# Kernel tuning notes

Hardware: AMD Instinct MI355X
Metric: run time of the kernel (lower is better)

Reference implementation:

```python
import jax, jax.numpy as jnp
import numpy as np

EPS = 1e-5
HEADS = 8
DIM_HEAD = 64
SCALE = DIM_HEAD ** -0.5
DEPTH = 4


def _layernorm(x, g, b):
    mu = jnp.mean(x, axis=-1, keepdims=True)
    var = jnp.var(x, axis=-1, keepdims=True)
    return (x - mu) * jax.lax.rsqrt(var + EPS) * g + b


def setup_inputs() -> dict:
    key = jax.random.key(0)
    ks = jax.random.split(key, 8)
    b, n, dim, mlp = 4, 1024, 512, 2048
    inner = HEADS * DIM_HEAD
    D = DEPTH
    s = 0.02  # realistic init scale
    return {
        "x": jax.random.normal(ks[0], (b, n, dim), jnp.float32),
        "ln1_g": jnp.ones((D, dim), jnp.float32),
        "ln1_b": jnp.zeros((D, dim), jnp.float32),
        "w_qkv": jax.random.normal(ks[1], (D, dim, 3 * inner), jnp.float32) * s,
        "reattn_w": jax.random.normal(ks[2], (D, HEADS, HEADS), jnp.float32),
        "rln_g": jnp.ones((D, HEADS), jnp.float32),
        "rln_b": jnp.zeros((D, HEADS), jnp.float32),
        "w_out": jax.random.normal(ks[3], (D, inner, dim), jnp.float32) * s,
        "b_out": jnp.zeros((D, dim), jnp.float32),
        "ln2_g": jnp.ones((D, dim), jnp.float32),
        "ln2_b": jnp.zeros((D, dim), jnp.float32),
        "w1": jax.random.normal(ks[4], (D, dim, mlp), jnp.float32) * s,
        "b1": jnp.zeros((D, mlp), jnp.float32),
        "w2": jax.random.normal(ks[5], (D, mlp, dim), jnp.float32) * s,
        "b2": jnp.zeros((D, dim), jnp.float32),
    }


def _attention(x, ln_g, ln_b, w_qkv, rw, rg, rb, w_out, b_out):
    b, n, dim = x.shape
    h, d = HEADS, DIM_HEAD
    hn = _layernorm(x, ln_g, ln_b)
    qkv = hn @ w_qkv  # [b, n, 3*h*d]
    q, k, v = jnp.split(qkv, 3, axis=-1)
    def to_heads(t):
        return t.reshape(b, n, h, d).transpose(0, 2, 1, 3)  # b h n d
    q, k, v = to_heads(q), to_heads(k), to_heads(v)
    dots = jnp.einsum('bhid,bhjd->bhij', q, k) * SCALE
    attn = jax.nn.softmax(dots, axis=-1)
    # cross-head re-attention mix
    attn = jnp.einsum('bhij,hg->bgij', attn, rw)
    # LayerNorm over the head axis (axis=1)
    mu = jnp.mean(attn, axis=1, keepdims=True)
    var = jnp.var(attn, axis=1, keepdims=True)
    attn = (attn - mu) * jax.lax.rsqrt(var + EPS)
    attn = attn * rg[None, :, None, None] + rb[None, :, None, None]
    out = jnp.einsum('bhij,bhjd->bhid', attn, v)
    out = out.transpose(0, 2, 1, 3).reshape(b, n, h * d)
    return out @ w_out + b_out


def _ffn(x, ln_g, ln_b, w1, b1, w2, b2):
    hn = _layernorm(x, ln_g, ln_b)
    hid = jax.nn.gelu(hn @ w1 + b1, approximate=False)
    return hid @ w2 + b2


def reference(x, ln1_g, ln1_b, w_qkv, reattn_w, rln_g, rln_b, w_out, b_out,
              ln2_g, ln2_b, w1, b1, w2, b2):
    for l in range(DEPTH):
        x = x + _attention(x, ln1_g[l], ln1_b[l], w_qkv[l], reattn_w[l],
                           rln_g[l], rln_b[l], w_out[l], b_out[l])
        x = x + _ffn(x, ln2_g[l], ln2_b[l], w1[l], b1[l], w2[l], b2[l])
        x = jnp.tanh(x)
    return x
```

## Files before the change

### kernel.cpp

```cpp
#include <hip/hip_runtime.h>
#include <math.h>

#define B 4
#define N 1024
#define DM 512
#define H 8
#define MLP 2048
#define TOK (B * N)
#define QKVW (3 * DM)
#define EPS 1e-5f
#define SCALE 0.125f

#define PS_HN  ((long)TOK * DM)
#define PS_WQ  ((long)QKVW * DM)

using short8 = __attribute__((ext_vector_type(8))) short;
using f32x4  = __attribute__((ext_vector_type(4))) float;
using u32x4  = __attribute__((ext_vector_type(4))) unsigned int;

__device__ __forceinline__ ushort f2b(float v) {
    unsigned int u = __builtin_bit_cast(unsigned int, v);
    u += 0x7fff + ((u >> 16) & 1);
    return (ushort)(u >> 16);
}
__device__ __forceinline__ float b2f(ushort u) {
    return __builtin_bit_cast(float, (unsigned int)u << 16);
}
__device__ __forceinline__ void split3(float v, ushort& h, ushort& l, ushort& q2) {
    h = f2b(v); float r1 = v - b2f(h);
    l = f2b(r1); q2 = f2b(r1 - b2f(l));
}
__device__ __forceinline__ void split_store8(f32x4 a0, f32x4 a1, char* base,
                                             int planeStride, int off) {
    short8 h8, l8, q8;
#pragma unroll
    for (int i = 0; i < 4; ++i) {
        ushort h, l, q;
        split3(a0[i], h, l, q);
        h8[i] = (short)h; l8[i] = (short)l; q8[i] = (short)q;
    }
#pragma unroll
    for (int i = 0; i < 4; ++i) {
        ushort h, l, q;
        split3(a1[i], h, l, q);
        h8[4 + i] = (short)h; l8[4 + i] = (short)l; q8[4 + i] = (short)q;
    }
    *(short8*)(base + off) = h8;
    *(short8*)(base + planeStride + off) = l8;
    *(short8*)(base + 2 * planeStride + off) = q8;
}

__global__ __launch_bounds__(256) void ln3_kernel(const float* __restrict__ x,
                                                  const float* __restrict__ g,
                                                  const float* __restrict__ bta,
                                                  ushort* __restrict__ out) {
    const int row = blockIdx.x;
    const int t = threadIdx.x;
    const float* xr = x + (size_t)row * DM;
    float v0 = xr[t], v1 = xr[t + 256];
    float s = v0 + v1, ss = v0 * v0 + v1 * v1;
    for (int o = 32; o; o >>= 1) {
        s += __shfl_down(s, o);
        ss += __shfl_down(ss, o);
    }
    __shared__ float ls[4], lss[4];
    const int wid = t >> 6, lane = t & 63;
    if (lane == 0) { ls[wid] = s; lss[wid] = ss; }
    __syncthreads();
    if (t == 0) {
        float S = ls[0] + ls[1] + ls[2] + ls[3];
        float SS = lss[0] + lss[1] + lss[2] + lss[3];
        float mu = S / DM;
        ls[0] = mu;
        lss[0] = SS / DM - mu * mu;
    }
    __syncthreads();
    const float mu = ls[0];
    const float r = rsqrtf(lss[0] + EPS);
    float o0 = (v0 - mu) * r * g[t] + bta[t];
    float o1 = (v1 - mu) * r * g[t + 256] + bta[t + 256];
    ushort h, l, q;
    size_t i0 = (size_t)row * DM + t;
    split3(o0, h, l, q);
    out[i0] = h; out[i0 + PS_HN] = l; out[i0 + 2 * PS_HN] = q;
    split3(o1, h, l, q);
    out[i0 + 256] = h; out[i0 + 256 + PS_HN] = l; out[i0 + 256 + 2 * PS_HN] = q;
}

__global__ __launch_bounds__(256) void wtrans_kernel(const float* __restrict__ W,
                                                     ushort* __restrict__ WT,
                                                     int K, int Nn, long ps) {
    __shared__ float ts[32][33];
    const int n0 = blockIdx.x * 32, k0 = blockIdx.y * 32;
    const int tx = threadIdx.x & 31, ty = threadIdx.x >> 5;
#pragma unroll
    for (int p = 0; p < 4; ++p)
        ts[ty + p * 8][tx] = W[(size_t)(k0 + ty + p * 8) * Nn + n0 + tx];
    __syncthreads();
#pragma unroll
    for (int p = 0; p < 4; ++p) {
        float v = ts[tx][ty + p * 8];
        ushort h, l, q;
        split3(v, h, l, q);
        size_t idx = (size_t)(n0 + ty + p * 8) * K + k0 + tx;
        WT[idx] = h;
        WT[idx + ps] = l;
        WT[idx + 2 * ps] = q;
    }
}

__global__ __launch_bounds__(256) void vtrans_kernel(const float* __restrict__ v,
                                                     float* __restrict__ vt) {
    const int z = blockIdx.z, b = z >> 3, h = z & 7;
    __shared__ float ts[32][33];
    const int j0 = blockIdx.x * 32, d0 = blockIdx.y * 32;
    const int tx = threadIdx.x & 31, ty = threadIdx.x >> 5;
#pragma unroll
    for (int p = 0; p < 4; ++p)
        ts[ty + p * 8][tx] =
            v[(size_t)(b * N + j0 + ty + p * 8) * DM + h * 64 + d0 + tx];
    __syncthreads();
#pragma unroll
    for (int p = 0; p < 4; ++p)
        vt[(size_t)((b * H + h) * 64 + d0 + ty + p * 8) * N + j0 + tx] =
            ts[tx][ty + p * 8];
}

template <int BM, int BN, int WR, int WC, int EPI, bool AF32, bool BF32, int ZDIV>
__global__ __launch_bounds__(256) void mm3_kernel(
    const void* __restrict__ Av, int sA, long pA, long zA,
    const void* __restrict__ Bv, int sB, long pB, long zB,
    const float* __restrict__ bias, const float* __restrict__ res,
    void* __restrict__ Cv, int sC, long zC, long zCk, int K, float scale) {
    constexpr int WM = BM / WR, WN = BN / WC;
    constexpr int FM = WM / 16, FN = WN / 16;
    constexpr int RA = BM / 64, RB = BN / 64;
    static_assert(!AF32 || RA <= 2, "AF32 assumes BM<=128");
    static_assert(!BF32 || RB <= 2, "BF32 assumes BN<=128");
    int bx, by, z;
    {
        const int gx = gridDim.x, gy = gridDim.y;
        const long nwg = (long)gx * gy * gridDim.z;
        long o = ((long)blockIdx.z * gy + blockIdx.y) * gx + blockIdx.x;
        if ((nwg & 7) == 0) { const long q = nwg >> 3; o = (o & 7) * q + (o >> 3); }
        bx = (int)(o % gx);
        const long r1 = o / gx;
        by = (int)(r1 % gy);
        z  = (int)(r1 / gy);
    }
    const int zo = z / ZDIV, zk = z % ZDIV;
    const ushort* A  = AF32 ? nullptr : (const ushort*)Av + (size_t)zo * zA;
    const float*  Af = AF32 ? (const float*)Av + (size_t)zo * zA : nullptr;
    const ushort* Bt = BF32 ? nullptr : (const ushort*)Bv + (size_t)zo * zB;
    const float*  Bf = BF32 ? (const float*)Bv + (size_t)zo * zB : nullptr;
    __shared__ char lds[3 * (BM + BN) * 64];
    char* Bbase = lds + 3 * BM * 64;
    const int t = threadIdx.x;
    const int lane = t & 63, w = t >> 6;
    const int wr = w / WC, wc = w % WC;
    const int m0 = by * BM, n0 = bx * BN;
    const int sr = t >> 2, skg = t & 3;
    const int off0 = sr * 64 + 16 * (skg ^ ((sr >> 1) & 3));

    f32x4 acc[FM][FN];
#pragma unroll
    for (int i = 0; i < FM; ++i)
#pragma unroll
        for (int j = 0; j < FN; ++j) acc[i][j] = (f32x4){0.f, 0.f, 0.f, 0.f};

    u32x4 cA[3][RA], nA[3][RA], cB[3][RB], nB[3][RB];
    f32x4 cAf[2 * RA], nAf[2 * RA], cBf[2 * RB], nBf[2 * RB];

    auto loadAll = [&](int KT, u32x4 (&DA)[3][RA], f32x4 (&DAf)[2 * RA],
                       u32x4 (&DB)[3][RB], f32x4 (&DBf)[2 * RB]) {
        if constexpr (AF32) {
#pragma unroll
            for (int p = 0; p < RA; ++p) {
                const float* s_ = Af + (size_t)(m0 + sr + p * 64) * sA + KT + skg * 8;
                DAf[2 * p] = *(const f32x4*)s_;
                DAf[2 * p + 1] = *(const f32x4*)(s_ + 4);
            }
        } else {
#pragma unroll
            for (int pl = 0; pl < 3; ++pl)
#pragma unroll
                for (int p = 0; p < RA; ++p)
                    DA[pl][p] = *(const u32x4*)(A + (size_t)pl * pA +
                        (size_t)(m0 + sr + p * 64) * sA + KT + skg * 8);
        }
        if constexpr (BF32) {
#pragma unroll
            for (int p = 0; p < RB; ++p) {
                const float* s_ = Bf + (size_t)(n0 + sr + p * 64) * sB + KT + skg * 8;
                DBf[2 * p] = *(const f32x4*)s_;
                DBf[2 * p + 1] = *(const f32x4*)(s_ + 4);
            }
        } else {
#pragma unroll
            for (int pl = 0; pl < 3; ++pl)
#pragma unroll
                for (int p = 0; p < RB; ++p)
                    DB[pl][p] = *(const u32x4*)(Bt + (size_t)pl * pB +
                        (size_t)(n0 + sr + p * 64) * sB + KT + skg * 8);
        }
    };
    auto storeAll = [&](u32x4 (&DA)[3][RA], f32x4 (&DAf)[2 * RA],
                        u32x4 (&DB)[3][RB], f32x4 (&DBf)[2 * RB]) {
        if constexpr (AF32) {
#pragma unroll
            for (int p = 0; p < RA; ++p)
                split_store8(DAf[2 * p], DAf[2 * p + 1], lds, BM * 64,
                             p * 4096 + off0);
        } else {
#pragma unroll
            for (int pl = 0; pl < 3; ++pl)
#pragma unroll
                for (int p = 0; p < RA; ++p)
                    *(u32x4*)(lds + pl * BM * 64 + p * 4096 + off0) = DA[pl][p];
        }
        if constexpr (BF32) {
#pragma unroll
            for (int p = 0; p < RB; ++p)
                split_store8(DBf[2 * p], DBf[2 * p + 1], Bbase, BN * 64,
                             p * 4096 + off0);
        } else {
#pragma unroll
            for (int pl = 0; pl < 3; ++pl)
#pragma unroll
                for (int p = 0; p < RB; ++p)
                    *(u32x4*)(Bbase + pl * BN * 64 + p * 4096 + off0) = DB[pl][p];
        }
    };

    const int Kc = K / ZDIV;
    const int kbeg = zk * Kc;
    loadAll(kbeg, cA, cAf, cB, cBf);
    for (int kt = kbeg; kt < kbeg + Kc; kt += 32) {
        __syncthreads();
        storeAll(cA, cAf, cB, cBf);
        if (kt + 32 < kbeg + Kc) loadAll(kt + 32, nA, nAf, nB, nBf);
        __syncthreads();
        short8 af[3][FM], bf[3][FN];
        const int kg = lane >> 4;
#pragma unroll
        for (int pl = 0; pl < 3; ++pl)
#pragma unroll
            for (int i = 0; i < FM; ++i) {
                const int r = wr * WM + i * 16 + (lane & 15);
                af[pl][i] = *(const short8*)(lds + pl * BM * 64 + r * 64 +
                                             16 * (kg ^ ((r >> 1) & 3)));
            }
#pragma unroll
        for (int pl = 0; pl < 3; ++pl)
#pragma unroll
            for (int j = 0; j < FN; ++j) {
                const int r = wc * WN + j * 16 + (lane & 15);
                bf[pl][j] = *(const short8*)(Bbase + pl * BN * 64 + r * 64 +
                                             16 * (kg ^ ((r >> 1) & 3)));
            }
#pragma unroll
        for (int i = 0; i < FM; ++i)
#pragma unroll
            for (int j = 0; j < FN; ++j)
#pragma unroll
                for (int s = 2; s >= 0; --s)
#pragma unroll
                    for (int ph = 0; ph <= 2; ++ph) {
                        const int pb = s - ph;
                        if (pb < 0 || pb > 2) continue;
                        acc[i][j] = __builtin_amdgcn_mfma_f32_16x16x32_bf16(
                            af[ph][i], bf[pb][j], acc[i][j], 0, 0, 0);
                    }
        if constexpr (AF32) {
#pragma unroll
            for (int p = 0; p < 2 * RA; ++p) cAf[p] = nAf[p];
        } else {
#pragma unroll
            for (int pl = 0; pl < 3; ++pl)
#pragma unroll
                for (int p = 0; p < RA; ++p) cA[pl][p] = nA[pl][p];
        }
        if constexpr (BF32) {
#pragma unroll
            for (int p = 0; p < 2 * RB; ++p) cBf[p] = nBf[p];
        } else {
#pragma unroll
            for (int pl = 0; pl < 3; ++pl)
#pragma unroll
                for (int p = 0; p < RB; ++p) cB[pl][p] = nB[pl][p];
        }
    }
    float* Cbase = (float*)Cv + (size_t)zo * zC + (size_t)zk * zCk;
#pragma unroll
    for (int i = 0; i < FM; ++i) {
#pragma unroll
        for (int j = 0; j < FN; ++j) {
            const int col = n0 + wc * WN + j * 16 + (lane & 15);
#pragma unroll
            for (int r4 = 0; r4 < 4; ++r4) {
                const int row = m0 + wr * WM + i * 16 + (lane >> 4) * 4 + r4;
                float v = acc[i][j][r4];
                if (EPI == 1) v *= scale;
                if (EPI == 2) {
                    v += bias[col];
                    v = 0.5f * v * (1.0f + erff(v * 0.70710678118654752f));
                }
                if (EPI == 3) {
                    if (col < 1024)
                        ((float*)Cv)[(size_t)row * 1024 + col] = v;
                    else
                        const_cast<float*>(res)[(size_t)row * 512 + col - 1024] = v;
                } else {
                    Cbase[(size_t)row * sC + col] = v;
                }
            }
        }
    }
}

template <int KS, int MODE>
__global__ __launch_bounds__(256) void red_kernel(const float* __restrict__ P,
                                                  long pstride,
                                                  const float* __restrict__ bias,
                                                  const float* __restrict__ X,
                                                  float* __restrict__ out) {
    const size_t e = ((size_t)blockIdx.x * 256 + threadIdx.x) * 4;
    f32x4 a = *(const f32x4*)(P + e);
#pragma unroll
    for (int k = 1; k < KS; ++k) {
        f32x4 pk = *(const f32x4*)(P + (size_t)k * pstride + e);
#pragma unroll
        for (int i = 0; i < 4; ++i) a[i] += pk[i];
    }
    if (MODE >= 1) {
        f32x4 xb = *(const f32x4*)(X + e);
        f32x4 bb = *(const f32x4*)(bias + (e & (DM - 1)));
#pragma unroll
        for (int i = 0; i < 4; ++i) {
            float r = xb[i] + a[i] + bb[i];
            a[i] = (MODE == 2) ? tanhf(r) : r;
        }
    }
    *(f32x4*)(out + e) = a;
}

__global__ __launch_bounds__(256) void softmax_mix_kernel(float* __restrict__ d,
                                                          const float* __restrict__ rw,
                                                          const float* __restrict__ rg,
                                                          const float* __restrict__ rb) {
    const int i = blockIdx.x;
    const int t = threadIdx.x;
    const int lane = t & 63, wid = t >> 6;
    __shared__ float red[4];
    __shared__ float srw[64], srg[8], srb[8];
    if (t < 64) srw[t] = rw[t];
    if (t < 8) { srg[t] = rg[t]; srb[t] = rb[t]; }
    f32x4 p[8];
#pragma unroll
    for (int h = 0; h < 8; ++h) {
        p[h] = ((const f32x4*)(d + ((size_t)h * 1024 + i) * 1024))[t];
        float lm = fmaxf(fmaxf(p[h][0], p[h][1]), fmaxf(p[h][2], p[h][3]));
        for (int o = 32; o; o >>= 1) lm = fmaxf(lm, __shfl_down(lm, o));
        __syncthreads();
        if (lane == 0) red[wid] = lm;
        __syncthreads();
        const float M = fmaxf(fmaxf(red[0], red[1]), fmaxf(red[2], red[3]));
        float ls = 0.f;
#pragma unroll
        for (int u = 0; u < 4; ++u) {
            p[h][u] = expf(p[h][u] - M);
            ls += p[h][u];
        }
        for (int o = 32; o; o >>= 1) ls += __shfl_down(ls, o);
        __syncthreads();
        if (lane == 0) red[wid] = ls;
        __syncthreads();
        const float inv = 1.0f / (red[0] + red[1] + red[2] + red[3]);
#pragma unroll
        for (int u = 0; u < 4; ++u) p[h][u] *= inv;
    }
    f32x4 mg[8];
#pragma unroll
    for (int g = 0; g < 8; ++g) {
#pragma unroll
        for (int u = 0; u < 4; ++u) {
            float acc = 0.f;
#pragma unroll
            for (int h = 0; h < 8; ++h) acc += p[h][u] * srw[h * 8 + g];
            mg[g][u] = acc;
        }
    }
#pragma unroll
    for (int u = 0; u < 4; ++u) {
        float mean = 0.f;
#pragma unroll
        for (int g = 0; g < 8; ++g) mean += mg[g][u];
        mean *= 0.125f;
        float var = 0.f;
#pragma unroll
        for (int g = 0; g < 8; ++g) { float dd = mg[g][u] - mean; var += dd * dd; }
        var *= 0.125f;
        const float rs = rsqrtf(var + EPS);
#pragma unroll
        for (int g = 0; g < 8; ++g) mg[g][u] = (mg[g][u] - mean) * rs * srg[g] + srb[g];
    }
#pragma unroll
    for (int g = 0; g < 8; ++g)
        ((f32x4*)(d + ((size_t)g * 1024 + i) * 1024))[t] = mg[g];
}

extern "C" void kernel_launch(void* const* d_in, const int* in_sizes, int n_in,
                              void* d_out, int out_size, void* d_ws, size_t ws_size,
                              hipStream_t stream) {
    const float* x_in  = (const float*)d_in[0];
    const float* ln1_g = (const float*)d_in[1];
    const float* ln1_b = (const float*)d_in[2];
    const float* w_qkv = (const float*)d_in[3];
    const float* re_w  = (const float*)d_in[4];
    const float* rln_g = (const float*)d_in[5];
    const float* rln_b = (const float*)d_in[6];
    const float* w_out = (const float*)d_in[7];
    const float* b_out = (const float*)d_in[8];
    const float* ln2_g = (const float*)d_in[9];
    const float* ln2_b = (const float*)d_in[10];
    const float* w1    = (const float*)d_in[11];
    const float* b1    = (const float*)d_in[12];
    const float* w2    = (const float*)d_in[13];
    const float* b2    = (const float*)d_in[14];

    char* wsb = (char*)d_ws;
    float*  X    = (float*)wsb;
    float*  QKf  = (float*)(wsb + (8ull << 20));
    float*  VTf  = (float*)(wsb + (24ull << 20));
    float*  D    = (float*)(wsb + (32ull << 20));
    float*  AO   = (float*)(wsb + (64ull << 20));
    float*  PVP  = (float*)(wsb + (72ull << 20));
    ushort* HN3  = (ushort*)(wsb + (32ull << 20));
    ushort* WQT  = (ushort*)(wsb + (44ull << 20));
    float*  Vf   = (float*)(wsb + (49ull << 20));
    ushort* WOT  = (ushort*)(wsb + (32ull << 20));
    float*  OPP  = (float*)(wsb + (34ull << 20));
    ushort* HN3f = (ushort*)(wsb + (8ull  << 20));
    ushort* W1T  = (ushort*)(wsb + (20ull << 20));
    ushort* W2T  = (ushort*)(wsb + (40ull << 20));
    float*  HIDf = (float*)(wsb + (48ull << 20));
    float*  FPP  = (float*)(wsb + (8ull  << 20));

    hipMemcpyAsync(X, x_in, sizeof(float) * (size_t)TOK * DM,
                   hipMemcpyDeviceToDevice, stream);

    for (int l = 0; l < 4; ++l) {
        ln3_kernel<<<TOK, 256, 0, stream>>>(X, ln1_g + l * DM, ln1_b + l * DM, HN3);
        wtrans_kernel<<<dim3(QKVW / 32, DM / 32), 256, 0, stream>>>(
            w_qkv + (size_t)l * DM * QKVW, WQT, DM, QKVW, PS_WQ);
        mm3_kernel<128, 128, 2, 2, 3, false, false, 1>
            <<<dim3(12, TOK / 128, 1), 256, 0, stream>>>(
            HN3, DM, PS_HN, 0, WQT, DM, PS_WQ, 0, nullptr, Vf,
            QKf, 1024, 0, 0, DM, 1.f);
        vtrans_kernel<<<dim3(N / 32, 2, B * H), 256, 0, stream>>>(Vf, VTf);

        for (int b = 0; b < B; ++b) {
            const float* qb = QKf + (size_t)b * N * 1024;
            mm3_kernel<128, 128, 2, 2, 1, true, true, 1>
                <<<dim3(8, 8, H), 256, 0, stream>>>(
                qb, 1024, 0, 64, qb + 512, 1024, 0, 64, nullptr, nullptr,
                D, 1024, (long)1024 * 1024, 0, 64, SCALE);
            softmax_mix_kernel<<<N, 256, 0, stream>>>(
                D, re_w + l * H * H, rln_g + l * H, rln_b + l * H);
            mm3_kernel<64, 64, 2, 2, 0, true, true, 4>
                <<<dim3(1, 16, H * 4), 256, 0, stream>>>(
                D, 1024, 0, (long)1024 * 1024,
                VTf + (size_t)b * H * 64 * N, 1024, 0, (long)64 * N,
                nullptr, nullptr,
                PVP, DM, 64, (long)N * DM, N, 1.f);
            red_kernel<4, 0><<<N * DM / 1024, 256, 0, stream>>>(
                PVP, (long)N * DM, nullptr, nullptr, AO + (size_t)b * N * DM);
        }
        wtrans_kernel<<<dim3(DM / 32, DM / 32), 256, 0, stream>>>(
            w_out + (size_t)l * DM * DM, WOT, DM, DM, (long)DM * DM);
        mm3_kernel<64, 128, 1, 4, 0, true, false, 2>
            <<<dim3(4, TOK / 64, 2), 256, 0, stream>>>(
            AO, DM, 0, 0, WOT, DM, (long)DM * DM, 0, nullptr, nullptr,
            OPP, DM, 0, (long)TOK * DM, DM, 1.f);
        red_kernel<2, 1><<<TOK * DM / 1024, 256, 0, stream>>>(
            OPP, (long)TOK * DM, b_out + l * DM, X, X);

        ln3_kernel<<<TOK, 256, 0, stream>>>(X, ln2_g + l * DM, ln2_b + l * DM, HN3f);
        wtrans_kernel<<<dim3(MLP / 32, DM / 32), 256, 0, stream>>>(
            w1 + (size_t)l * DM * MLP, W1T, DM, MLP, (long)MLP * DM);
        mm3_kernel<128, 128, 2, 2, 2, false, false, 1>
            <<<dim3(MLP / 128, TOK / 128, 1), 256, 0, stream>>>(
            HN3f, DM, PS_HN, 0, W1T, DM, (long)MLP * DM, 0, b1 + l * MLP, nullptr,
            HIDf, MLP, 0, 0, DM, 1.f);
        wtrans_kernel<<<dim3(DM / 32, MLP / 32), 256, 0, stream>>>(
            w2 + (size_t)l * MLP * DM, W2T, MLP, DM, (long)DM * MLP);
        mm3_kernel<128, 128, 2, 2, 0, true, false, 4>
            <<<dim3(4, TOK / 128, 4), 256, 0, stream>>>(
            HIDf, MLP, 0, 0, W2T, MLP, (long)DM * MLP, 0, nullptr, nullptr,
            FPP, DM, 0, (long)TOK * DM, MLP, 1.f);
        float* outp = (l == 3) ? (float*)d_out : X;
        red_kernel<4, 2><<<TOK * DM / 1024, 256, 0, stream>>>(
            FPP, (long)TOK * DM, b2 + l * DM, X, outp);
    }
}
```

Baseline: 1.739 ms.

## Fuse split-K reduction with residual, tanh and following LayerNorm

Adds a redln kernel that sums the split-K partials, adds bias and residual (with optional tanh), writes X, and then computes the next LayerNorm and its 3-way bf16 split in the same pass. This removes the separate ln3 launches after the attention-output and FFN-output reductions, which saves a full re-read of X per layer. The workspace buffers are rearranged to avoid the new aliasing. The P·V GEMM tile is also enlarged from 64 to 128 rows, giving half as many blocks.

```diff
diff --git a/kernel.cpp b/kernel.cpp
--- a/kernel.cpp
+++ b/kernel.cpp
@@ -85,6 +85,55 @@
     out[i0] = h; out[i0 + PS_HN] = l; out[i0 + 2 * PS_HN] = q;
     split3(o1, h, l, q);
     out[i0 + 256] = h; out[i0 + 256 + PS_HN] = l; out[i0 + 256 + 2 * PS_HN] = q;
+}
+
+template <int KS, bool TANH>
+__global__ __launch_bounds__(256) void redln_kernel(
+    const float* __restrict__ P, long pstride, const float* __restrict__ bias,
+    const float* __restrict__ X, float* __restrict__ Xout,
+    const float* __restrict__ g, const float* __restrict__ bta,
+    ushort* __restrict__ out) {
+    const int row = blockIdx.x;
+    const int t = threadIdx.x;
+    const size_t e0 = (size_t)row * DM + t;
+    const size_t e1 = e0 + 256;
+    float a0 = P[e0], a1 = P[e1];
+#pragma unroll
+    for (int k = 1; k < KS; ++k) {
+        a0 += P[(size_t)k * pstride + e0];
+        a1 += P[(size_t)k * pstride + e1];
+    }
+    float v0 = X[e0] + a0 + bias[t];
+    float v1 = X[e1] + a1 + bias[t + 256];
+    if (TANH) { v0 = tanhf(v0); v1 = tanhf(v1); }
+    Xout[e0] = v0;
+    Xout[e1] = v1;
+    float s = v0 + v1, ss = v0 * v0 + v1 * v1;
+    for (int o = 32; o; o >>= 1) {
+        s += __shfl_down(s, o);
+        ss += __shfl_down(ss, o);
+    }
+    __shared__ float ls[4], lss[4];
+    const int wid = t >> 6, lane = t & 63;
+    if (lane == 0) { ls[wid] = s; lss[wid] = ss; }
+    __syncthreads();
+    if (t == 0) {
+        float S = ls[0] + ls[1] + ls[2] + ls[3];
+        float SS = lss[0] + lss[1] + lss[2] + lss[3];
+        float mu = S / DM;
+        ls[0] = mu;
+        lss[0] = SS / DM - mu * mu;
+    }
+    __syncthreads();
+    const float mu = ls[0];
+    const float r = rsqrtf(lss[0] + EPS);
+    float o0 = (v0 - mu) * r * g[t] + bta[t];
+    float o1 = (v1 - mu) * r * g[t + 256] + bta[t + 256];
+    ushort h, l, q;
+    split3(o0, h, l, q);
+    out[e0] = h; out[e0 + PS_HN] = l; out[e0 + 2 * PS_HN] = q;
+    split3(o1, h, l, q);
+    out[e1] = h; out[e1 + PS_HN] = l; out[e1 + 2 * PS_HN] = q;
 }
 
 __global__ __launch_bounds__(256) void wtrans_kernel(const float* __restrict__ W,
@@ -431,26 +480,27 @@
     char* wsb = (char*)d_ws;
     float*  X    = (float*)wsb;
     float*  QKf  = (float*)(wsb + (8ull << 20));
+    ushort* HN3f = (ushort*)(wsb + (8ull  << 20));
+    float*  FPP  = (float*)(wsb + (8ull  << 20));
+    ushort* W1T  = (ushort*)(wsb + (20ull << 20));
     float*  VTf  = (float*)(wsb + (24ull << 20));
     float*  D    = (float*)(wsb + (32ull << 20));
+    float*  Vf   = (float*)(wsb + (32ull << 20));
+    ushort* WOT  = (ushort*)(wsb + (32ull << 20));
+    float*  OPP  = (float*)(wsb + (34ull << 20));
+    ushort* W2T  = (ushort*)(wsb + (40ull << 20));
+    ushort* WQT  = (ushort*)(wsb + (40ull << 20));
+    ushort* HN3  = (ushort*)(wsb + (48ull << 20));
+    float*  HIDf = (float*)(wsb + (48ull << 20));
     float*  AO   = (float*)(wsb + (64ull << 20));
     float*  PVP  = (float*)(wsb + (72ull << 20));
-    ushort* HN3  = (ushort*)(wsb + (32ull << 20));
-    ushort* WQT  = (ushort*)(wsb + (44ull << 20));
-    float*  Vf   = (float*)(wsb + (49ull << 20));
-    ushort* WOT  = (ushort*)(wsb + (32ull << 20));
-    float*  OPP  = (float*)(wsb + (34ull << 20));
-    ushort* HN3f = (ushort*)(wsb + (8ull  << 20));
-    ushort* W1T  = (ushort*)(wsb + (20ull << 20));
-    ushort* W2T  = (ushort*)(wsb + (40ull << 20));
-    float*  HIDf = (float*)(wsb + (48ull << 20));
-    float*  FPP  = (float*)(wsb + (8ull  << 20));
 
     hipMemcpyAsync(X, x_in, sizeof(float) * (size_t)TOK * DM,
                    hipMemcpyDeviceToDevice, stream);
 
     for (int l = 0; l < 4; ++l) {
-        ln3_kernel<<<TOK, 256, 0, stream>>>(X, ln1_g + l * DM, ln1_b + l * DM, HN3);
+        if (l == 0)
+            ln3_kernel<<<TOK, 256, 0, stream>>>(X, ln1_g, ln1_b, HN3);
         wtrans_kernel<<<dim3(QKVW / 32, DM / 32), 256, 0, stream>>>(
             w_qkv + (size_t)l * DM * QKVW, WQT, DM, QKVW, PS_WQ);
         mm3_kernel<128, 128, 2, 2, 3, false, false, 1>
@@ -467,8 +517,8 @@
                 D, 1024, (long)1024 * 1024, 0, 64, SCALE);
             softmax_mix_kernel<<<N, 256, 0, stream>>>(
                 D, re_w + l * H * H, rln_g + l * H, rln_b + l * H);
-            mm3_kernel<64, 64, 2, 2, 0, true, true, 4>
-                <<<dim3(1, 16, H * 4), 256, 0, stream>>>(
+            mm3_kernel<128, 64, 2, 2, 0, true, true, 4>
+                <<<dim3(1, 8, H * 4), 256, 0, stream>>>(
                 D, 1024, 0, (long)1024 * 1024,
                 VTf + (size_t)b * H * 64 * N, 1024, 0, (long)64 * N,
                 nullptr, nullptr,
@@ -482,10 +532,10 @@
             <<<dim3(4, TOK / 64, 2), 256, 0, stream>>>(
             AO, DM, 0, 0, WOT, DM, (long)DM * DM, 0, nullptr, nullptr,
             OPP, DM, 0, (long)TOK * DM, DM, 1.f);
-        red_kernel<2, 1><<<TOK * DM / 1024, 256, 0, stream>>>(
-            OPP, (long)TOK * DM, b_out + l * DM, X, X);
-
-        ln3_kernel<<<TOK, 256, 0, stream>>>(X, ln2_g + l * DM, ln2_b + l * DM, HN3f);
+        redln_kernel<2, false><<<TOK, 256, 0, stream>>>(
+            OPP, (long)TOK * DM, b_out + l * DM, X, X,
+            ln2_g + l * DM, ln2_b + l * DM, HN3f);
+
         wtrans_kernel<<<dim3(MLP / 32, DM / 32), 256, 0, stream>>>(
             w1 + (size_t)l * DM * MLP, W1T, DM, MLP, (long)MLP * DM);
         mm3_kernel<128, 128, 2, 2, 2, false, false, 1>
@@ -498,8 +548,13 @@
             <<<dim3(4, TOK / 128, 4), 256, 0, stream>>>(
             HIDf, MLP, 0, 0, W2T, MLP, (long)DM * MLP, 0, nullptr, nullptr,
             FPP, DM, 0, (long)TOK * DM, MLP, 1.f);
-        float* outp = (l == 3) ? (float*)d_out : X;
-        red_kernel<4, 2><<<TOK * DM / 1024, 256, 0, stream>>>(
-            FPP, (long)TOK * DM, b2 + l * DM, X, outp);
-    }
-}
+        if (l < 3) {
+            redln_kernel<4, true><<<TOK, 256, 0, stream>>>(
+                FPP, (long)TOK * DM, b2 + l * DM, X, X,
+                ln1_g + (l + 1) * DM, ln1_b + (l + 1) * DM, HN3);
+        } else {
+            red_kernel<4, 2><<<TOK * DM / 1024, 256, 0, stream>>>(
+                FPP, (long)TOK * DM, b2 + l * DM, X, (float*)d_out);
+        }
+    }
+}
```

Measured after the change: 1.725 ms. About the same (-0.8%).
